# Performance work log

Hardware: AMD Instinct MI355X
Metric: run time of the kernel (lower is better)

The kernel has to match this reference:

```python
import jax, jax.numpy as jnp
import numpy as np

N_NODES = 100000
N_EDGES = 1600000
D_FEAT = 48
N_LAYERS = 3  # GCN(n_layers=3) builds exactly 3 GraphConv layers


def setup_inputs() -> dict:
    key = jax.random.key(0)
    k1, k2, k3 = jax.random.split(key, 3)
    features = jax.random.normal(k1, (N_NODES, D_FEAT), dtype=jnp.float32)
    src = jax.random.randint(k2, (N_EDGES,), 0, N_NODES, dtype=jnp.int32)
    dst = jax.random.randint(k3, (N_EDGES,), 0, N_NODES, dtype=jnp.int32)
    return {"features": features, "src": src, "dst": dst}


def reference(features, src, dst):
    # GraphConv(norm='none', weight=False, bias=False): h_v = sum_{u->v} h_u, then activation.
    # Layers 0..N_LAYERS-2 apply relu; the final layer has no activation.
    h = features
    for i in range(N_LAYERS):
        msgs = h[src]  # gather source features per edge: [E, D]
        h = jax.ops.segment_sum(msgs, dst, num_segments=N_NODES)  # scatter-add to dst
        if i < N_LAYERS - 1:
            h = jax.nn.relu(h)
    return h
```

## Files before the change

kernel.cpp:

```cpp
#include <hip/hip_runtime.h>

#define D 48
#define BSH 8
#define BN 256
#define NBMAX 400
#define CH 256
#define CAPT 5120
#define LOUTSZ 6400
#define PB 6400

typedef float v2f __attribute__((ext_vector_type(2)));
typedef unsigned int u32x2_t __attribute__((ext_vector_type(2)));
typedef unsigned int u32x4_t __attribute__((ext_vector_type(4)));
typedef float f32x4_t __attribute__((ext_vector_type(4)));

#if defined(__has_builtin)
#if __has_builtin(__builtin_amdgcn_cvt_pk_f32_fp8)
#define HAVE_HW_FP8 1
#endif
#if __has_builtin(__builtin_amdgcn_cvt_pk_fp8_f32)
#define HAVE_HW_FP8ENC 1
#endif
#endif

static __device__ inline void nt_store_u2(uint2* p, unsigned int x, unsigned int y) {
    u32x2_t v; v.x = x; v.y = y;
    __builtin_nontemporal_store(v, (u32x2_t*)p);
}
static __device__ inline void nt_store_u4(uint4* p, unsigned int x, unsigned int y,
                                          unsigned int z, unsigned int w) {
    u32x4_t v; v.x = x; v.y = y; v.z = z; v.w = w;
    __builtin_nontemporal_store(v, (u32x4_t*)p);
}
static __device__ inline void nt_store_f4(float* p, float x, float y, float z, float w) {
    f32x4_t v; v.x = x; v.y = y; v.z = z; v.w = w;
    __builtin_nontemporal_store(v, (f32x4_t*)p);
}

static __device__ inline unsigned int f2bf_rne(float x) {
    unsigned int u = __float_as_uint(x);
    return (u + 0x7FFFu + ((u >> 16) & 1u)) >> 16;
}
static __device__ inline unsigned int pack2(float lo, float hi) {
    return f2bf_rne(lo) | (f2bf_rne(hi) << 16);
}
static __device__ inline float bf_lo(unsigned int u) { return __uint_as_float(u << 16); }
static __device__ inline float bf_hi(unsigned int u) { return __uint_as_float(u & 0xFFFF0000u); }

static __device__ inline unsigned int f2fp8(float x) {
    unsigned int u = __float_as_uint(x);
    unsigned int s = (u >> 24) & 0x80u;
    unsigned int e = (u >> 23) & 0xFFu;
    unsigned int m = u & 0x7FFFFFu;
    if (e < 121u) return s;
    unsigned int m2 = m + 0x7FFFFu + ((m >> 20) & 1u);
    unsigned int carry = m2 >> 23;
    unsigned int e2 = e - 120u + carry;
    unsigned int b = s | (e2 << 3) | ((m2 >> 20) & 7u);
    if (e2 > 15u || (b & 0x7Fu) == 0x7Fu) b = s | 0x7Eu;
    return b;
}
static __device__ inline float fp8_dec(unsigned int b) {
    unsigned int bits = ((b & 0x80u) << 24) | (((b & 0x7Fu) << 20) + (120u << 23));
    float v = __uint_as_float(bits);
    return ((b & 0x7Fu) != 0u) ? v : 0.0f;
}
static __device__ inline unsigned int packfp8x4(float a, float b, float c, float d) {
#if HAVE_HW_FP8ENC
    int w = __builtin_amdgcn_cvt_pk_fp8_f32(a, b, 0, false);
    w = __builtin_amdgcn_cvt_pk_fp8_f32(c, d, w, true);
    return (unsigned int)w;
#else
    return f2fp8(a) | (f2fp8(b) << 8) | (f2fp8(c) << 16) | (f2fp8(d) << 24);
#endif
}


__global__ void k_fscat(const int* __restrict__ src, const int* __restrict__ dst,
                        const float* __restrict__ feat,
                        uint2* __restrict__ featq, uint2* __restrict__ h1q,
                        uint4* __restrict__ featb, int* __restrict__ btot,
                        int* __restrict__ stage, int E, int NB, int CHE, int N) {
    int t = threadIdx.x;
    if (blockIdx.x < CH) {
        int c = blockIdx.x;
        __shared__ int h[NBMAX];
        __shared__ int curl[NBMAX];
        for (int b = t; b < NB; b += 1024) h[b] = 0;
        __syncthreads();
        int lo = c * CHE, hi = min(lo + CHE, E);
        for (int i = lo + t; i < hi; i += 1024)
            atomicAdd(&h[dst[i] >> BSH], 1);
        __syncthreads();
        for (int b = t; b < NB; b += 1024)
            curl[b] = b * CAPT + atomicAdd(&btot[b], h[b]);
        __syncthreads();
        for (int i = lo + t; i < hi; i += 1024) {
            int s = src[i], d = dst[i];
            int bkt = d >> BSH;
            int p = atomicAdd(&curl[bkt], 1);
            if (p < (bkt + 1) * CAPT)
                stage[p] = ((d & (BN - 1)) << 17) | s;
        }
    } else {
        if (blockIdx.x == CH && t < 8) {
            nt_store_u2(&h1q[(size_t)N * 8 + t], 0u, 0u);
            nt_store_u4(&featb[(size_t)N * 8 + t], 0u, 0u, 0u, 0u);
        }
        const float4* f4 = (const float4*)feat;
        int total = (N + 1) * 8;
        int i = (blockIdx.x - CH) * 1024 + t;
        int stride = 256 * 1024;
        for (; i < total; i += stride) {
            int node = i >> 3, cc = i & 7;
            unsigned int vx = 0u, vy = 0u;
            if (cc < 6 && node < N) {
                float4 a = f4[node * 12 + 2 * cc];
                float4 b = f4[node * 12 + 2 * cc + 1];
                vx = f2fp8(a.x) | (f2fp8(a.y) << 8) | (f2fp8(a.z) << 16) | (f2fp8(a.w) << 24);
                vy = f2fp8(b.x) | (f2fp8(b.y) << 8) | (f2fp8(b.z) << 16) | (f2fp8(b.w) << 24);
            }
            nt_store_u2(&featq[i], vx, vy);
        }
    }
}


__global__ void k_build(const int* __restrict__ stage, const int* __restrict__ btot,
                        int* __restrict__ row_ptr, int* __restrict__ trips,
                        int* __restrict__ esrc, int N, int NB) {
    int b = blockIdx.x;
    int t = threadIdx.x;
    __shared__ int lbuf[CAPT];
    __shared__ int lout[LOUTSZ];
    __shared__ int hist[BN];
    __shared__ int cur[BN];
    __shared__ int wt[4];
    __shared__ int stot;
    int base = b * CAPT;
    int cnt = min(btot[b], CAPT);
    hist[t] = 0;
    __syncthreads();
    for (int i = t; i < cnt; i += 256) {
        int v = __builtin_nontemporal_load(stage + base + i);
        lbuf[i] = v;
        atomicAdd(&hist[v >> 17], 1);
    }
    __syncthreads();
    int orig = hist[t];
    int pc = (orig + 7) & ~7;
    int w = t >> 6, ln = t & 63;
    int x = pc;
#pragma unroll
    for (int off = 1; off < 64; off <<= 1) {
        int u = __shfl_up(x, off);
        if (ln >= off) x += u;
    }
    if (ln == 63) wt[w] = x;
    __syncthreads();
    if (t == 0) {
        int a = 0;
        for (int k = 0; k < 4; k++) { int tmp = wt[k]; wt[k] = a; a += tmp; }
    }
    __syncthreads();
    int ppre = x - pc + wt[w];
    cur[t] = ppre;
    int node = (b << BSH) + t;
    if (node < N) {
        __builtin_nontemporal_store(b * PB + ppre, row_ptr + node);
        __builtin_nontemporal_store(pc >> 3, trips + node);
    }
    for (int k = orig; k < pc; k++) lout[ppre + k] = N;
    if (t == 255) stot = ppre + pc;
    __syncthreads();
    for (int i = t; i < cnt; i += 256) {
        int v = lbuf[i];
        int p = atomicAdd(&cur[v >> 17], 1);
        lout[p] = v & 0x1FFFF;
    }
    __syncthreads();
    int ptot = stot;
    for (int i = t; i < ptot; i += 256)
        __builtin_nontemporal_store(lout[i], esrc + b * PB + i);
}


#if HAVE_HW_FP8
#define DEC8(q) do { \
        v2f p0 = __builtin_amdgcn_cvt_pk_f32_fp8((int)(q).x, false); \
        v2f p1 = __builtin_amdgcn_cvt_pk_f32_fp8((int)(q).x, true); \
        v2f p2 = __builtin_amdgcn_cvt_pk_f32_fp8((int)(q).y, false); \
        v2f p3 = __builtin_amdgcn_cvt_pk_f32_fp8((int)(q).y, true); \
        a0 += p0.x; a1 += p0.y; a2 += p1.x; a3 += p1.y; \
        a4 += p2.x; a5 += p2.y; a6 += p3.x; a7 += p3.y; } while (0)
#else
#define DEC8(q) do { \
        a0 += fp8_dec((q).x & 0xFFu); a1 += fp8_dec(((q).x >> 8) & 0xFFu); \
        a2 += fp8_dec(((q).x >> 16) & 0xFFu); a3 += fp8_dec((q).x >> 24); \
        a4 += fp8_dec((q).y & 0xFFu); a5 += fp8_dec(((q).y >> 8) & 0xFFu); \
        a6 += fp8_dec(((q).y >> 16) & 0xFFu); a7 += fp8_dec((q).y >> 24); } while (0)
#endif

template <int OUTBF16>
__global__ void k_pullq(const uint2* __restrict__ hin, void* __restrict__ hout,
                        const int* __restrict__ row_ptr, const int* __restrict__ trips,
                        const int* __restrict__ esrc, int n) {
    int grp = threadIdx.x >> 4;
    int lane = threadIdx.x & 15;
    int side = lane >> 3;
    int sub = lane & 7;
    int node = blockIdx.x * 16 + grp;
    if (node >= n) return;
    int j = row_ptr[node];
    int nt = trips[node];
    float a0 = 0.f, a1 = 0.f, a2 = 0.f, a3 = 0.f, a4 = 0.f, a5 = 0.f, a6 = 0.f, a7 = 0.f;
    if (nt > 0) {
        int4 s4 = *(const int4*)(esrc + j + 4 * side);
        for (; nt > 0; --nt) {
            uint2 q0 = hin[(size_t)s4.x * 8 + sub];
            uint2 q1 = hin[(size_t)s4.y * 8 + sub];
            uint2 q2 = hin[(size_t)s4.z * 8 + sub];
            uint2 q3 = hin[(size_t)s4.w * 8 + sub];
            j += 8;
            int4 n4 = *(const int4*)(esrc + j + 4 * side);
            DEC8(q0); DEC8(q1); DEC8(q2); DEC8(q3);
            s4 = n4;
        }
    }
    a0 += __shfl_xor(a0, 8); a1 += __shfl_xor(a1, 8);
    a2 += __shfl_xor(a2, 8); a3 += __shfl_xor(a3, 8);
    a4 += __shfl_xor(a4, 8); a5 += __shfl_xor(a5, 8);
    a6 += __shfl_xor(a6, 8); a7 += __shfl_xor(a7, 8);
    a0 = fmaxf(a0, 0.f); a1 = fmaxf(a1, 0.f); a2 = fmaxf(a2, 0.f); a3 = fmaxf(a3, 0.f);
    a4 = fmaxf(a4, 0.f); a5 = fmaxf(a5, 0.f); a6 = fmaxf(a6, 0.f); a7 = fmaxf(a7, 0.f);
    if (side != 0) return;
    if (OUTBF16) {
        nt_store_u4((uint4*)hout + (size_t)node * 8 + sub,
                    pack2(a0, a1), pack2(a2, a3), pack2(a4, a5), pack2(a6, a7));
    } else {
        nt_store_u2((uint2*)hout + (size_t)node * 8 + sub,
                    packfp8x4(a0, a1, a2, a3), packfp8x4(a4, a5, a6, a7));
    }
}
#undef DEC8


__global__ void k_pull(const uint4* __restrict__ hin, float* __restrict__ hout,
                       const int* __restrict__ row_ptr, const int* __restrict__ trips,
                       const int* __restrict__ esrc, int n) {
    int grp = threadIdx.x >> 4;
    int lane = threadIdx.x & 15;
    int side = lane >> 3;
    int sub = lane & 7;
    int node = blockIdx.x * 16 + grp;
    if (node >= n) return;
    int j = row_ptr[node];
    int nt = trips[node];
    float a0 = 0.f, a1 = 0.f, a2 = 0.f, a3 = 0.f, a4 = 0.f, a5 = 0.f, a6 = 0.f, a7 = 0.f;
    if (nt > 0) {
        int4 s4 = *(const int4*)(esrc + j + 4 * side);
        for (; nt > 0; --nt) {
            uint4 q0 = hin[(size_t)s4.x * 8 + sub];
            uint4 q1 = hin[(size_t)s4.y * 8 + sub];
            uint4 q2 = hin[(size_t)s4.z * 8 + sub];
            uint4 q3 = hin[(size_t)s4.w * 8 + sub];
            j += 8;
            int4 n4 = *(const int4*)(esrc + j + 4 * side);
            a0 += bf_lo(q0.x); a1 += bf_hi(q0.x); a2 += bf_lo(q0.y); a3 += bf_hi(q0.y);
            a4 += bf_lo(q0.z); a5 += bf_hi(q0.z); a6 += bf_lo(q0.w); a7 += bf_hi(q0.w);
            a0 += bf_lo(q1.x); a1 += bf_hi(q1.x); a2 += bf_lo(q1.y); a3 += bf_hi(q1.y);
            a4 += bf_lo(q1.z); a5 += bf_hi(q1.z); a6 += bf_lo(q1.w); a7 += bf_hi(q1.w);
            a0 += bf_lo(q2.x); a1 += bf_hi(q2.x); a2 += bf_lo(q2.y); a3 += bf_hi(q2.y);
            a4 += bf_lo(q2.z); a5 += bf_hi(q2.z); a6 += bf_lo(q2.w); a7 += bf_hi(q2.w);
            a0 += bf_lo(q3.x); a1 += bf_hi(q3.x); a2 += bf_lo(q3.y); a3 += bf_hi(q3.y);
            a4 += bf_lo(q3.z); a5 += bf_hi(q3.z); a6 += bf_lo(q3.w); a7 += bf_hi(q3.w);
            s4 = n4;
        }
    }
    a0 += __shfl_xor(a0, 8); a1 += __shfl_xor(a1, 8);
    a2 += __shfl_xor(a2, 8); a3 += __shfl_xor(a3, 8);
    a4 += __shfl_xor(a4, 8); a5 += __shfl_xor(a5, 8);
    a6 += __shfl_xor(a6, 8); a7 += __shfl_xor(a7, 8);
    if (side != 0) return;
    if (sub < 6) {
        float* o = hout + (size_t)node * D + 8 * sub;
        nt_store_f4(o, a0, a1, a2, a3);
        nt_store_f4(o + 4, a4, a5, a6, a7);
    }
}

extern "C" void kernel_launch(void* const* d_in, const int* in_sizes, int n_in,
                              void* d_out, int out_size, void* d_ws, size_t ws_size,
                              hipStream_t stream) {
    const float* feat = (const float*)d_in[0];
    const int* src = (const int*)d_in[1];
    const int* dst = (const int*)d_in[2];
    int N = in_sizes[0] / D;
    int E = in_sizes[1];
    int NB = (N + BN - 1) >> BSH;
    int CHE = (E + CH - 1) / CH;

    char* ws = (char*)d_ws;
    int*   btot    = (int*)(ws);
    int*   row_ptr = (int*)(ws + ((size_t)640 << 10));
    int*   trips   = (int*)(ws + ((size_t)1152 << 10));
    int*   esrc    = (int*)(ws + ((size_t)2 << 20));
    uint2* featq   = (uint2*)(ws + ((size_t)13 << 20));
    uint4* featb   = (uint4*)(ws + ((size_t)20 << 20));
    int*   stage   = (int*)(ws + ((size_t)33 << 20));
    uint2* h1q     = (uint2*)(ws + ((size_t)42 << 20));

    hipMemsetAsync(btot, 0, (size_t)NB * sizeof(int), stream);

    k_fscat<<<CH + 256, 1024, 0, stream>>>(src, dst, feat, featq, h1q, featb, btot, stage, E, NB, CHE, N);
    k_build<<<NB, 256, 0, stream>>>(stage, btot, row_ptr, trips, esrc, N, NB);

    int pg = (N + 15) / 16;
    k_pullq<0><<<pg, 256, 0, stream>>>(featq, h1q, row_ptr, trips, esrc, N);
    k_pullq<1><<<pg, 256, 0, stream>>>(h1q, featb, row_ptr, trips, esrc, N);
    k_pull<<<pg, 256, 0, stream>>>(featb, (float*)d_out, row_ptr, trips, esrc, N);
}
```

Before: 179.0 us.

## Fuse three pull layers into one persistent kernel with grid barriers

Replaces the three per-layer pull kernel launches with one persistent kernel of 1024 blocks that loops over node groups and separates the layers with atomic grid-wide barriers. The layer-2 bf16 buffer is also packed at 6 uint4 per node instead of 8, removing padding from the final gather. This removes launch gaps and tail effects between layers but depends on all 1024 blocks being co-resident, and it adds barrier spin cost and lower parallelism per layer.

```diff
diff --git a/kernel.cpp b/kernel.cpp
--- a/kernel.cpp
+++ b/kernel.cpp
@@ -8,6 +8,7 @@
 #define CAPT 5120
 #define LOUTSZ 6400
 #define PB 6400
+#define GRID 1024
 
 typedef float v2f __attribute__((ext_vector_type(2)));
 typedef unsigned int u32x2_t __attribute__((ext_vector_type(2)));
@@ -75,11 +76,23 @@
 #endif
 }
 
+static __device__ inline void gridbar(int* b) {
+    __syncthreads();
+    if (threadIdx.x == 0) {
+        __threadfence();
+        __hip_atomic_fetch_add(b, 1, __ATOMIC_ACQ_REL, __HIP_MEMORY_SCOPE_AGENT);
+        while (__hip_atomic_load(b, __ATOMIC_ACQUIRE, __HIP_MEMORY_SCOPE_AGENT) < GRID)
+            __builtin_amdgcn_s_sleep(2);
+        __threadfence();
+    }
+    __syncthreads();
+}
+
 
 __global__ void k_fscat(const int* __restrict__ src, const int* __restrict__ dst,
                         const float* __restrict__ feat,
                         uint2* __restrict__ featq, uint2* __restrict__ h1q,
-                        uint4* __restrict__ featb, int* __restrict__ btot,
+                        uint4* __restrict__ h2p, int* __restrict__ btot,
                         int* __restrict__ stage, int E, int NB, int CHE, int N) {
     int t = threadIdx.x;
     if (blockIdx.x < CH) {
@@ -103,9 +116,9 @@
                 stage[p] = ((d & (BN - 1)) << 17) | s;
         }
     } else {
-        if (blockIdx.x == CH && t < 8) {
-            nt_store_u2(&h1q[(size_t)N * 8 + t], 0u, 0u);
-            nt_store_u4(&featb[(size_t)N * 8 + t], 0u, 0u, 0u, 0u);
+        if (blockIdx.x == CH) {
+            if (t < 8) nt_store_u2(&h1q[(size_t)N * 8 + t], 0u, 0u);
+            if (t < 6) nt_store_u4(&h2p[(size_t)N * 6 + t], 0u, 0u, 0u, 0u);
         }
         const float4* f4 = (const float4*)feat;
         int total = (N + 1) * 8;
@@ -201,93 +214,108 @@
         a6 += fp8_dec(((q).y >> 16) & 0xFFu); a7 += fp8_dec((q).y >> 24); } while (0)
 #endif
 
-template <int OUTBF16>
-__global__ void k_pullq(const uint2* __restrict__ hin, void* __restrict__ hout,
-                        const int* __restrict__ row_ptr, const int* __restrict__ trips,
-                        const int* __restrict__ esrc, int n) {
+#define FP8_GATHER(HIN) do { \
+    int j = row_ptr[node]; \
+    int ntr = trips[node]; \
+    if (ntr > 0) { \
+        int4 s4 = *(const int4*)(esrc + j + 4 * side); \
+        for (; ntr > 0; --ntr) { \
+            uint2 q0 = (HIN)[(size_t)s4.x * 8 + sub]; \
+            uint2 q1 = (HIN)[(size_t)s4.y * 8 + sub]; \
+            uint2 q2 = (HIN)[(size_t)s4.z * 8 + sub]; \
+            uint2 q3 = (HIN)[(size_t)s4.w * 8 + sub]; \
+            j += 8; \
+            int4 n4 = *(const int4*)(esrc + j + 4 * side); \
+            DEC8(q0); DEC8(q1); DEC8(q2); DEC8(q3); \
+            s4 = n4; \
+        } \
+    } \
+    a0 += __shfl_xor(a0, 8); a1 += __shfl_xor(a1, 8); \
+    a2 += __shfl_xor(a2, 8); a3 += __shfl_xor(a3, 8); \
+    a4 += __shfl_xor(a4, 8); a5 += __shfl_xor(a5, 8); \
+    a6 += __shfl_xor(a6, 8); a7 += __shfl_xor(a7, 8); \
+    a0 = fmaxf(a0, 0.f); a1 = fmaxf(a1, 0.f); a2 = fmaxf(a2, 0.f); a3 = fmaxf(a3, 0.f); \
+    a4 = fmaxf(a4, 0.f); a5 = fmaxf(a5, 0.f); a6 = fmaxf(a6, 0.f); a7 = fmaxf(a7, 0.f); \
+} while (0)
+
+__global__ __launch_bounds__(256, 4)
+void k_pull3(const uint2* __restrict__ featq, uint2* __restrict__ h1q,
+             uint4* __restrict__ h2p, float* __restrict__ out,
+             const int* __restrict__ row_ptr, const int* __restrict__ trips,
+             const int* __restrict__ esrc, int n, int* __restrict__ bar) {
     int grp = threadIdx.x >> 4;
     int lane = threadIdx.x & 15;
     int side = lane >> 3;
     int sub = lane & 7;
-    int node = blockIdx.x * 16 + grp;
-    if (node >= n) return;
-    int j = row_ptr[node];
-    int nt = trips[node];
-    float a0 = 0.f, a1 = 0.f, a2 = 0.f, a3 = 0.f, a4 = 0.f, a5 = 0.f, a6 = 0.f, a7 = 0.f;
-    if (nt > 0) {
-        int4 s4 = *(const int4*)(esrc + j + 4 * side);
-        for (; nt > 0; --nt) {
-            uint2 q0 = hin[(size_t)s4.x * 8 + sub];
-            uint2 q1 = hin[(size_t)s4.y * 8 + sub];
-            uint2 q2 = hin[(size_t)s4.z * 8 + sub];
-            uint2 q3 = hin[(size_t)s4.w * 8 + sub];
-            j += 8;
-            int4 n4 = *(const int4*)(esrc + j + 4 * side);
-            DEC8(q0); DEC8(q1); DEC8(q2); DEC8(q3);
-            s4 = n4;
-        }
-    }
-    a0 += __shfl_xor(a0, 8); a1 += __shfl_xor(a1, 8);
-    a2 += __shfl_xor(a2, 8); a3 += __shfl_xor(a3, 8);
-    a4 += __shfl_xor(a4, 8); a5 += __shfl_xor(a5, 8);
-    a6 += __shfl_xor(a6, 8); a7 += __shfl_xor(a7, 8);
-    a0 = fmaxf(a0, 0.f); a1 = fmaxf(a1, 0.f); a2 = fmaxf(a2, 0.f); a3 = fmaxf(a3, 0.f);
-    a4 = fmaxf(a4, 0.f); a5 = fmaxf(a5, 0.f); a6 = fmaxf(a6, 0.f); a7 = fmaxf(a7, 0.f);
-    if (side != 0) return;
-    if (OUTBF16) {
-        nt_store_u4((uint4*)hout + (size_t)node * 8 + sub,
-                    pack2(a0, a1), pack2(a2, a3), pack2(a4, a5), pack2(a6, a7));
-    } else {
-        nt_store_u2((uint2*)hout + (size_t)node * 8 + sub,
-                    packfp8x4(a0, a1, a2, a3), packfp8x4(a4, a5, a6, a7));
+    int pg = (n + 15) >> 4;
+
+    for (int g = blockIdx.x; g < pg; g += GRID) {
+        int node = g * 16 + grp;
+        if (node < n) {
+            float a0 = 0.f, a1 = 0.f, a2 = 0.f, a3 = 0.f, a4 = 0.f, a5 = 0.f, a6 = 0.f, a7 = 0.f;
+            FP8_GATHER(featq);
+            if (side == 0)
+                nt_store_u2(&h1q[(size_t)node * 8 + sub],
+                            packfp8x4(a0, a1, a2, a3), packfp8x4(a4, a5, a6, a7));
+        }
+    }
+    gridbar(&bar[0]);
+
+    for (int g = blockIdx.x; g < pg; g += GRID) {
+        int node = g * 16 + grp;
+        if (node < n) {
+            float a0 = 0.f, a1 = 0.f, a2 = 0.f, a3 = 0.f, a4 = 0.f, a5 = 0.f, a6 = 0.f, a7 = 0.f;
+            FP8_GATHER(h1q);
+            if (side == 0 && sub < 6)
+                nt_store_u4(&h2p[(size_t)node * 6 + sub],
+                            pack2(a0, a1), pack2(a2, a3), pack2(a4, a5), pack2(a6, a7));
+        }
+    }
+    gridbar(&bar[1]);
+
+    for (int g = blockIdx.x; g < pg; g += GRID) {
+        int node = g * 16 + grp;
+        if (node < n) {
+            int j = row_ptr[node];
+            int ntr = trips[node];
+            float a0 = 0.f, a1 = 0.f, a2 = 0.f, a3 = 0.f, a4 = 0.f, a5 = 0.f, a6 = 0.f, a7 = 0.f;
+            if (ntr > 0) {
+                int4 s4 = *(const int4*)(esrc + j + 4 * side);
+                for (; ntr > 0; --ntr) {
+                    uint4 q0 = make_uint4(0u, 0u, 0u, 0u), q1 = q0, q2 = q0, q3 = q0;
+                    if (sub < 6) {
+                        q0 = h2p[(size_t)s4.x * 6 + sub];
+                        q1 = h2p[(size_t)s4.y * 6 + sub];
+                        q2 = h2p[(size_t)s4.z * 6 + sub];
+                        q3 = h2p[(size_t)s4.w * 6 + sub];
+                    }
+                    j += 8;
+                    int4 n4 = *(const int4*)(esrc + j + 4 * side);
+                    a0 += bf_lo(q0.x); a1 += bf_hi(q0.x); a2 += bf_lo(q0.y); a3 += bf_hi(q0.y);
+                    a4 += bf_lo(q0.z); a5 += bf_hi(q0.z); a6 += bf_lo(q0.w); a7 += bf_hi(q0.w);
+                    a0 += bf_lo(q1.x); a1 += bf_hi(q1.x); a2 += bf_lo(q1.y); a3 += bf_hi(q1.y);
+                    a4 += bf_lo(q1.z); a5 += bf_hi(q1.z); a6 += bf_lo(q1.w); a7 += bf_hi(q1.w);
+                    a0 += bf_lo(q2.x); a1 += bf_hi(q2.x); a2 += bf_lo(q2.y); a3 += bf_hi(q2.y);
+                    a4 += bf_lo(q2.z); a5 += bf_hi(q2.z); a6 += bf_lo(q2.w); a7 += bf_hi(q2.w);
+                    a0 += bf_lo(q3.x); a1 += bf_hi(q3.x); a2 += bf_lo(q3.y); a3 += bf_hi(q3.y);
+                    a4 += bf_lo(q3.z); a5 += bf_hi(q3.z); a6 += bf_lo(q3.w); a7 += bf_hi(q3.w);
+                    s4 = n4;
+                }
+            }
+            a0 += __shfl_xor(a0, 8); a1 += __shfl_xor(a1, 8);
+            a2 += __shfl_xor(a2, 8); a3 += __shfl_xor(a3, 8);
+            a4 += __shfl_xor(a4, 8); a5 += __shfl_xor(a5, 8);
+            a6 += __shfl_xor(a6, 8); a7 += __shfl_xor(a7, 8);
+            if (side == 0 && sub < 6) {
+                float* o = out + (size_t)node * D + 8 * sub;
+                nt_store_f4(o, a0, a1, a2, a3);
+                nt_store_f4(o + 4, a4, a5, a6, a7);
+            }
+        }
     }
 }
 #undef DEC8
-
-
-__global__ void k_pull(const uint4* __restrict__ hin, float* __restrict__ hout,
-                       const int* __restrict__ row_ptr, const int* __restrict__ trips,
-                       const int* __restrict__ esrc, int n) {
-    int grp = threadIdx.x >> 4;
-    int lane = threadIdx.x & 15;
-    int side = lane >> 3;
-    int sub = lane & 7;
-    int node = blockIdx.x * 16 + grp;
-    if (node >= n) return;
-    int j = row_ptr[node];
-    int nt = trips[node];
-    float a0 = 0.f, a1 = 0.f, a2 = 0.f, a3 = 0.f, a4 = 0.f, a5 = 0.f, a6 = 0.f, a7 = 0.f;
-    if (nt > 0) {
-        int4 s4 = *(const int4*)(esrc + j + 4 * side);
-        for (; nt > 0; --nt) {
-            uint4 q0 = hin[(size_t)s4.x * 8 + sub];
-            uint4 q1 = hin[(size_t)s4.y * 8 + sub];
-            uint4 q2 = hin[(size_t)s4.z * 8 + sub];
-            uint4 q3 = hin[(size_t)s4.w * 8 + sub];
-            j += 8;
-            int4 n4 = *(const int4*)(esrc + j + 4 * side);
-            a0 += bf_lo(q0.x); a1 += bf_hi(q0.x); a2 += bf_lo(q0.y); a3 += bf_hi(q0.y);
-            a4 += bf_lo(q0.z); a5 += bf_hi(q0.z); a6 += bf_lo(q0.w); a7 += bf_hi(q0.w);
-            a0 += bf_lo(q1.x); a1 += bf_hi(q1.x); a2 += bf_lo(q1.y); a3 += bf_hi(q1.y);
-            a4 += bf_lo(q1.z); a5 += bf_hi(q1.z); a6 += bf_lo(q1.w); a7 += bf_hi(q1.w);
-            a0 += bf_lo(q2.x); a1 += bf_hi(q2.x); a2 += bf_lo(q2.y); a3 += bf_hi(q2.y);
-            a4 += bf_lo(q2.z); a5 += bf_hi(q2.z); a6 += bf_lo(q2.w); a7 += bf_hi(q2.w);
-            a0 += bf_lo(q3.x); a1 += bf_hi(q3.x); a2 += bf_lo(q3.y); a3 += bf_hi(q3.y);
-            a4 += bf_lo(q3.z); a5 += bf_hi(q3.z); a6 += bf_lo(q3.w); a7 += bf_hi(q3.w);
-            s4 = n4;
-        }
-    }
-    a0 += __shfl_xor(a0, 8); a1 += __shfl_xor(a1, 8);
-    a2 += __shfl_xor(a2, 8); a3 += __shfl_xor(a3, 8);
-    a4 += __shfl_xor(a4, 8); a5 += __shfl_xor(a5, 8);
-    a6 += __shfl_xor(a6, 8); a7 += __shfl_xor(a7, 8);
-    if (side != 0) return;
-    if (sub < 6) {
-        float* o = hout + (size_t)node * D + 8 * sub;
-        nt_store_f4(o, a0, a1, a2, a3);
-        nt_store_f4(o + 4, a4, a5, a6, a7);
-    }
-}
+#undef FP8_GATHER
 
 extern "C" void kernel_launch(void* const* d_in, const int* in_sizes, int n_in,
                               void* d_out, int out_size, void* d_ws, size_t ws_size,
@@ -302,21 +330,19 @@
 
     char* ws = (char*)d_ws;
     int*   btot    = (int*)(ws);
+    int*   bar     = (int*)(ws + 2048);
     int*   row_ptr = (int*)(ws + ((size_t)640 << 10));
     int*   trips   = (int*)(ws + ((size_t)1152 << 10));
     int*   esrc    = (int*)(ws + ((size_t)2 << 20));
     uint2* featq   = (uint2*)(ws + ((size_t)13 << 20));
-    uint4* featb   = (uint4*)(ws + ((size_t)20 << 20));
+    uint4* h2p     = (uint4*)(ws + ((size_t)20 << 20));
     int*   stage   = (int*)(ws + ((size_t)33 << 20));
     uint2* h1q     = (uint2*)(ws + ((size_t)42 << 20));
 
-    hipMemsetAsync(btot, 0, (size_t)NB * sizeof(int), stream);
-
-    k_fscat<<<CH + 256, 1024, 0, stream>>>(src, dst, feat, featq, h1q, featb, btot, stage, E, NB, CHE, N);
+    hipMemsetAsync(ws, 0, 4096, stream);
+
+    k_fscat<<<CH + 256, 1024, 0, stream>>>(src, dst, feat, featq, h1q, h2p, btot, stage, E, NB, CHE, N);
     k_build<<<NB, 256, 0, stream>>>(stage, btot, row_ptr, trips, esrc, N, NB);
-
-    int pg = (N + 15) / 16;
-    k_pullq<0><<<pg, 256, 0, stream>>>(featq, h1q, row_ptr, trips, esrc, N);
-    k_pullq<1><<<pg, 256, 0, stream>>>(h1q, featb, row_ptr, trips, esrc, N);
-    k_pull<<<pg, 256, 0, stream>>>(featb, (float*)d_out, row_ptr, trips, esrc, N);
-}
+    k_pull3<<<GRID, 256, 0, stream>>>(featq, h1q, h2p, (float*)d_out,
+                                      row_ptr, trips, esrc, N, bar);
+}
```

New measurement: 538.7 us. 3.01x slower.
